# Kernel tuning notes

Measured on AMD Instinct MI355X. Metric: run time of the kernel, lower is better.

The kernel has to match this reference:

```python
import jax, jax.numpy as jnp
import numpy as np

EPS = 1e-6
INV_T = 100.0
STEPS = 7  # eval_steps


def setup_inputs() -> dict:
    key = jax.random.key(0)
    k1, k2 = jax.random.split(key)
    B, C, H, W, R = 8, 512, 128, 128, 64
    x = jax.random.uniform(k1, (B, C, H, W), dtype=jnp.float32)
    bases = jax.random.uniform(k2, (B, C, R), dtype=jnp.float32)
    # _build_bases: F.normalize(bases, dim=1) -> L2 normalize over D
    bases = bases / jnp.maximum(jnp.linalg.norm(bases, axis=1, keepdims=True), 1e-12)
    return {"x": x, "bases": bases}


def _nmf(xf, bases):
    # xf: [B, D, N], bases: [B, D, R]
    # coef init: softmax(inv_t * x^T @ bases) over R
    coef = jax.nn.softmax(INV_T * jnp.einsum('bdn,bdr->bnr', xf, bases), axis=-1)

    def step(carry, _):
        bases, coef = carry
        # multiplicative update for coef: coef * (x^T B) / (coef (B^T B))
        num = jnp.einsum('bdn,bdr->bnr', xf, bases)          # [B,N,R]
        den = coef @ (jnp.swapaxes(bases, 1, 2) @ bases)      # [B,N,R]
        coef = coef * num / (den + EPS)
        # multiplicative update for bases: B * (x coef) / (B (coef^T coef))
        num = jnp.einsum('bdn,bnr->bdr', xf, coef)            # [B,D,R]
        den = bases @ (jnp.swapaxes(coef, 1, 2) @ coef)       # [B,D,R]
        bases = bases * num / (den + EPS)
        return (bases, coef), None

    (bases, coef), _ = jax.lax.scan(step, (bases, coef), None, length=STEPS)
    # compute_coef: one final coef update
    num = jnp.einsum('bdn,bdr->bnr', xf, bases)
    den = coef @ (jnp.swapaxes(bases, 1, 2) @ bases)
    coef = coef * num / (den + EPS)
    return bases, coef


def reference(x, bases):
    B, C, H, W = x.shape
    N = H * W
    xf = x.reshape(B, C, N)  # S=1, D=C
    bases, coef = _nmf(xf, bases)
    out = jnp.einsum('bdr,bnr->bdn', bases, coef)  # bases @ coef^T
    return out.reshape(B, C, H, W)
```

## Files before the change

kernel.cpp:

```cpp
#include <hip/hip_runtime.h>
#include <cstdint>
#include <cstddef>

namespace {

constexpr int B_ = 8;
constexpr int D_ = 512;
constexpr int N_ = 16384;
constexpr int R_ = 64;
constexpr float EPS_ = 1e-6f;
constexpr float INVT_ = 100.0f;

typedef __attribute__((ext_vector_type(4))) float f32x4;
typedef __attribute__((ext_vector_type(8))) short s16x8;
typedef __attribute__((ext_vector_type(4))) short s16x4;

#define MFMA16(A, Bv, C) __builtin_amdgcn_mfma_f32_16x16x32_bf16(A, Bv, C, 0, 0, 0)

#define VMW(n) asm volatile("s_waitcnt vmcnt(" #n ")" ::: "memory")
#define LGKM0 asm volatile("s_waitcnt lgkmcnt(0)" ::: "memory")
#define SCHEDB __builtin_amdgcn_sched_barrier(0)
#define BARRIER do { SCHEDB; __builtin_amdgcn_s_barrier(); SCHEDB; } while (0)

typedef __attribute__((address_space(3))) unsigned int lds_u32_t;
typedef const __attribute__((address_space(1))) unsigned int glb_u32_t;

__device__ __forceinline__ void gl2lds16(const void* g, void* l) {
    __builtin_amdgcn_global_load_lds((glb_u32_t*)g, (lds_u32_t*)l, 16, 0, 0);
}

__device__ __forceinline__ unsigned short f2bf(float x) {
    unsigned int u = __float_as_uint(x);
    return (unsigned short)((u + 0x7fffu + ((u >> 16) & 1u)) >> 16);
}
__device__ __forceinline__ float bf2f(unsigned short u) {
    return __uint_as_float(((unsigned int)u) << 16);
}
__device__ __forceinline__ s16x8 ld8(const unsigned short* p) {
    return *reinterpret_cast<const s16x8*>(p);
}

__device__ __forceinline__ void stage16(const unsigned short* __restrict__ rowbase,
        size_t rstride_elems, unsigned short* __restrict__ buf, int w, int lane) {
#pragma unroll
    for (int i = 0; i < 4; ++i) {
        int r = w * 4 + i;
        const char* src = reinterpret_cast<const char*>(rowbase + (size_t)r * rstride_elems)
                        + ((lane << 4) ^ ((r & 7) << 4));
        gl2lds16(src, reinterpret_cast<char*>(buf) + r * 1024);
    }
}
__device__ __forceinline__ s16x8 read_t16(const unsigned short* buf, int row, int ks, int h4) {
    return *reinterpret_cast<const s16x8*>(reinterpret_cast<const char*>(buf)
        + row * 1024 + ((ks * 64 + h4 * 16) ^ ((row & 7) << 4)));
}
__device__ __forceinline__ void stage_c16(const unsigned short* __restrict__ cnr_n0,
        unsigned short* __restrict__ buf, int w, int lane) {
    int h = w & 1;
    int row = h * 8 + (lane >> 3);
    const char* src = reinterpret_cast<const char*>(cnr_n0 + (size_t)row * R_)
                    + ((((lane & 7) ^ (row & 7))) << 4);
    gl2lds16(src, reinterpret_cast<char*>(buf) + h * 1024);
}
__device__ __forceinline__ s16x8 read_c16(const unsigned short* buf, int row, int ks, int h4) {
    return *reinterpret_cast<const s16x8*>(reinterpret_cast<const char*>(buf)
        + row * 128 + ((ks * 64 + h4 * 16) ^ ((row & 7) << 4)));
}
__device__ __forceinline__ float read_c_scalar(const unsigned short* buf, int row, int r) {
    return bf2f(*reinterpret_cast<const unsigned short*>(
        reinterpret_cast<const char*>(buf) + row * 128 + ((r * 2) ^ ((row & 7) << 4))));
}

__global__ __launch_bounds__(256) void k_convert(const float* __restrict__ X,
        unsigned short* __restrict__ Xhi, unsigned short* __restrict__ XThi,
        unsigned short* __restrict__ XTlo, int have_lo) {
    __shared__ f32x4 lds4[64 * 16];
    int id = blockIdx.x;
    int nblk = id & 255, dblk = (id >> 8) & 7, b = id >> 11;
    int t = threadIdx.x;
    int d = t >> 2, c0 = (t & 3) * 16;
    const float* Xb = X + ((size_t)b * D_ + dblk * 64) * N_ + (size_t)nblk * 64;
    f32x4 v[4];
#pragma unroll
    for (int i = 0; i < 4; ++i)
        v[i] = *reinterpret_cast<const f32x4*>(Xb + (size_t)d * N_ + c0 + 4 * i);
    {
        int swz = (d ^ (d >> 3)) & 7;
#pragma unroll
        for (int i = 0; i < 4; ++i)
            lds4[d * 16 + ((((t & 3) << 2) + i) ^ swz)] = v[i];
    }
    {
        int dfull = dblk * 64 + d;
        int n0 = nblk * 64 + c0;
        unsigned short* dst = Xhi + (size_t)b * D_ * N_
                            + ((size_t)((dfull >> 4) * 32 + (n0 >> 9))) * 8192
                            + (dfull & 15) * 512 + (n0 & 511);
        s16x8 h0, h1;
#pragma unroll
        for (int k = 0; k < 8; ++k) {
            h0[k] = (short)f2bf(v[k >> 2][k & 3]);
            h1[k] = (short)f2bf(v[2 + (k >> 2)][k & 3]);
        }
        *reinterpret_cast<s16x8*>(dst) = h0;
        *reinterpret_cast<s16x8*>(dst + 8) = h1;
    }
    __syncthreads();
    {
        int n = t >> 2;
        const float* L = reinterpret_cast<const float*>(lds4);
        s16x8 h0, h1, l0, l1;
#pragma unroll
        for (int k = 0; k < 16; ++k) {
            int r = c0 + k;
            int sz = (r ^ (r >> 3)) & 7;
            float a = L[r * 64 + ((((n >> 2) ^ sz) << 2) | (n & 3))];
            unsigned short ha = f2bf(a);
            unsigned short la = f2bf(a - bf2f(ha));
            if (k < 8) { h0[k] = (short)ha; l0[k] = (short)la; }
            else       { h1[k - 8] = (short)ha; l1[k - 8] = (short)la; }
        }
        size_t off = ((size_t)b * N_ + nblk * 64 + n) * D_ + dblk * 64 + c0;
        *reinterpret_cast<s16x8*>(XThi + off) = h0;
        *reinterpret_cast<s16x8*>(XThi + off + 8) = h1;
        if (have_lo) {
            *reinterpret_cast<s16x8*>(XTlo + off) = l0;
            *reinterpret_cast<s16x8*>(XTlo + off + 8) = l1;
        }
    }
}

__global__ __launch_bounds__(256) void k_ginit(const float* __restrict__ Bin,
        float* __restrict__ bases, unsigned short* __restrict__ BThi,
        unsigned short* __restrict__ BTlo) {
    __shared__ float lds[64][65];
    int id = blockIdx.x, dblk = id & 7, b = id >> 3;
    int t = threadIdx.x, tn = t & 63, tq = t >> 6;
    const float* Bb = Bin + ((size_t)b * D_ + dblk * 64) * R_;
    float* bb = bases + ((size_t)b * D_ + dblk * 64) * R_;
#pragma unroll
    for (int i = 0; i < 16; ++i) {
        int d = i * 4 + tq;
        float v = Bb[d * R_ + tn];
        lds[d][tn] = v;
        bb[d * R_ + tn] = v;
    }
    __syncthreads();
#pragma unroll
    for (int i = 0; i < 16; ++i) {
        int r = i * 4 + tq;
        float v = lds[tn][r];
        unsigned short hi = f2bf(v);
        size_t off = ((size_t)b * R_ + r) * D_ + dblk * 64 + tn;
        BThi[off] = hi;
        BTlo[off] = f2bf(v - bf2f(hi));
    }
}

__global__ __launch_bounds__(256) void k_gram(const unsigned short* __restrict__ BT,
        unsigned short* __restrict__ G, float* __restrict__ Hf, int zf) {
    int b = blockIdx.x;
    int t = threadIdx.x, lane = t & 63, w = t >> 6;
    int m16 = lane & 15, h4 = lane >> 4;
    if (zf) {
        float* Hz = Hf + (size_t)b * 4096;
#pragma unroll
        for (int i = 0; i < 4; ++i)
            *reinterpret_cast<f32x4*>(Hz + i * 1024 + t * 4) = (f32x4){0.f, 0.f, 0.f, 0.f};
    }
    const unsigned short* BTb = BT + (size_t)b * R_ * D_;
    f32x4 acc[4];
#pragma unroll
    for (int j = 0; j < 4; ++j) acc[j] = (f32x4){0.f, 0.f, 0.f, 0.f};
#pragma unroll
    for (int k0 = 0; k0 < D_; k0 += 32) {
        int kg = k0 + (h4 << 3);
        s16x8 frag[4];
#pragma unroll
        for (int j = 0; j < 4; ++j)
            frag[j] = ld8(BTb + (size_t)(j * 16 + m16) * D_ + kg);
        s16x8 fw = ld8(BTb + (size_t)(w * 16 + m16) * D_ + kg);
#pragma unroll
        for (int j = 0; j < 4; ++j) acc[j] = MFMA16(fw, frag[j], acc[j]);
    }
    unsigned short* Gb = G + (size_t)b * R_ * R_;
#pragma unroll
    for (int j = 0; j < 4; ++j)
#pragma unroll
        for (int q = 0; q < 4; ++q) {
            int r1 = 16 * w + (h4 << 2) + q;
            Gb[r1 * R_ + 16 * j + m16] = f2bf(acc[j][q]);
        }
}

template <int LO>
__global__ __launch_bounds__(256, 2) void k_init(const unsigned short* __restrict__ XThi,
        const unsigned short* __restrict__ XTlo, const unsigned short* __restrict__ BThi,
        const unsigned short* __restrict__ BTlo, const unsigned short* __restrict__ G,
        unsigned short* __restrict__ CTb, unsigned short* __restrict__ Cnr) {
    __shared__ __align__(16) unsigned short xhbuf[2][16 * 512];
    __shared__ __align__(16) unsigned short xlbuf[LO ? 2 : 1][16 * 512];
    __shared__ __align__(16) unsigned short ldsc[16 * 64];
    __shared__ float red[2][4][16];
    int id = blockIdx.x, blk = id & 63, b = id >> 6;
    int t = threadIdx.x, lane = t & 63, w = t >> 6;
    int m16 = lane & 15, h4 = lane >> 4;
    const unsigned short* XTb = XThi + (size_t)b * N_ * D_;
    const unsigned short* XLb = XTlo + (size_t)b * N_ * D_;
    const unsigned short* BThb = BThi + (size_t)b * R_ * D_;
    const unsigned short* BTlb = BTlo + (size_t)b * R_ * D_;
    const unsigned short* Gb = G + (size_t)b * R_ * R_;
    unsigned short* CTbb = CTb + (size_t)b * R_ * N_;
    unsigned short* Cnrb = Cnr + (size_t)b * N_ * R_;
    s16x8 abh[16], abl[16], g[2];
#pragma unroll
    for (int ks = 0; ks < 16; ++ks) {
        size_t off = (size_t)(w * 16 + m16) * D_ + ks * 32 + h4 * 8;
        abh[ks] = ld8(BThb + off);
        abl[ks] = ld8(BTlb + off);
    }
#pragma unroll
    for (int ks = 0; ks < 2; ++ks)
        g[ks] = ld8(Gb + (size_t)(w * 16 + m16) * R_ + ks * 32 + h4 * 8);
    SCHEDB;
    stage16(XTb + (size_t)(blk * 16 + 0) * 16 * D_, D_, xhbuf[0], w, lane);
    if (LO) stage16(XLb + (size_t)(blk * 16 + 0) * 16 * D_, D_, xlbuf[0], w, lane);
    stage16(XTb + (size_t)(blk * 16 + 1) * 16 * D_, D_, xhbuf[1], w, lane);
    if (LO) stage16(XLb + (size_t)(blk * 16 + 1) * 16 * D_, D_, xlbuf[1], w, lane);
    SCHEDB;

    int swz = (m16 & 7) << 4;
    char* crow = reinterpret_cast<char*>(ldsc) + m16 * 128;

    for (int tt = 0; tt < 16; ++tt) {
        int cur = tt & 1;
        int n0 = (blk * 16 + tt) * 16;
        if (LO) {
            if (tt == 0) VMW(8);
            else if (tt == 15) VMW(5);
            else VMW(13);
        } else {
            if (tt == 0) VMW(4);
            else if (tt == 15) VMW(5);
            else VMW(9);
        }
        BARRIER;
        const unsigned short* xh = xhbuf[cur];
        const unsigned short* xl = xlbuf[LO ? cur : 0];
        f32x4 acc = (f32x4){0.f, 0.f, 0.f, 0.f};
#pragma unroll
        for (int ks = 0; ks < 16; ++ks) {
            s16x8 bh = read_t16(xh, m16, ks, h4);
            acc = MFMA16(abh[ks], bh, acc);
            acc = MFMA16(abl[ks], bh, acc);
            if (LO) {
                s16x8 bl = read_t16(xl, m16, ks, h4);
                acc = MFMA16(abh[ks], bl, acc);
            }
        }
        float mx = fmaxf(fmaxf(acc[0], acc[1]), fmaxf(acc[2], acc[3]));
        mx = fmaxf(mx, __shfl_xor(mx, 16));
        mx = fmaxf(mx, __shfl_xor(mx, 32));
        if (lane < 16) red[0][w][m16] = mx;
        LGKM0; BARRIER;
        mx = fmaxf(fmaxf(red[0][0][m16], red[0][1][m16]),
                   fmaxf(red[0][2][m16], red[0][3][m16]));
        float p[4], ss = 0.f;
#pragma unroll
        for (int q = 0; q < 4; ++q) {
            p[q] = __expf(INVT_ * (acc[q] - mx));
            ss += p[q];
        }
        ss += __shfl_xor(ss, 16);
        ss += __shfl_xor(ss, 32);
        if (lane < 16) red[1][w][m16] = ss;
        LGKM0; BARRIER;
        ss = red[1][0][m16] + red[1][1][m16] + red[1][2][m16] + red[1][3][m16];
        float inv = 1.f / ss;
#pragma unroll
        for (int q = 0; q < 4; ++q) {
            int r = w * 16 + h4 * 4 + q;
            *reinterpret_cast<unsigned short*>(crow + ((r * 2) ^ swz)) = f2bf(p[q] * inv);
        }
        LGKM0; BARRIER;
        f32x4 dacc = (f32x4){0.f, 0.f, 0.f, 0.f};
#pragma unroll
        for (int ks = 0; ks < 2; ++ks) {
            s16x8 bf = *reinterpret_cast<const s16x8*>(crow + ((ks * 64 + h4 * 16) ^ swz));
            dacc = MFMA16(g[ks], bf, dacc);
        }
        s16x4 cn;
        float c1v[4];
#pragma unroll
        for (int q = 0; q < 4; ++q) {
            c1v[q] = p[q] * inv * acc[q] / (dacc[q] + EPS_);
            cn[q] = (short)f2bf(c1v[q]);
        }
        LGKM0; BARRIER;
        SCHEDB;
#pragma unroll
        for (int q = 0; q < 4; ++q)
            CTbb[(size_t)(w * 16 + h4 * 4 + q) * N_ + n0 + m16] = f2bf(c1v[q]);
        *reinterpret_cast<s16x4*>(Cnrb + (size_t)(n0 + m16) * R_ + w * 16 + h4 * 4) = cn;
        SCHEDB;
        if (tt + 2 < 16) {
            stage16(XTb + (size_t)(blk * 16 + tt + 2) * 16 * D_, D_, xhbuf[cur], w, lane);
            if (LO) stage16(XLb + (size_t)(blk * 16 + tt + 2) * 16 * D_, D_, xlbuf[cur], w, lane);
        }
        SCHEDB;
    }
}

__global__ __launch_bounds__(256, 4) void k_cu(const unsigned short* __restrict__ XThi,
        const unsigned short* __restrict__ BThi, const unsigned short* __restrict__ G,
        unsigned short* __restrict__ CTb, unsigned short* __restrict__ Cnr) {
    __shared__ __align__(16) unsigned short xbuf[2][16 * 512];
    __shared__ __align__(16) unsigned short cbuf[2][16 * 64];
    int id = blockIdx.x, blk = id & 127, b = id >> 7;
    int t = threadIdx.x, lane = t & 63, w = t >> 6;
    int m16 = lane & 15, h4 = lane >> 4;
    const unsigned short* XTb = XThi + (size_t)b * N_ * D_;
    const unsigned short* BTb = BThi + (size_t)b * R_ * D_;
    const unsigned short* Gb = G + (size_t)b * R_ * R_;
    unsigned short* CTbb = CTb + (size_t)b * R_ * N_;
    unsigned short* Cnrb = Cnr + (size_t)b * N_ * R_;
    s16x8 abt[16], g[2];
#pragma unroll
    for (int ks = 0; ks < 16; ++ks)
        abt[ks] = ld8(BTb + (size_t)(w * 16 + m16) * D_ + ks * 32 + h4 * 8);
#pragma unroll
    for (int ks = 0; ks < 2; ++ks)
        g[ks] = ld8(Gb + (size_t)(w * 16 + m16) * R_ + ks * 32 + h4 * 8);
    SCHEDB;
    stage16(XTb + (size_t)(blk * 8 + 0) * 16 * D_, D_, xbuf[0], w, lane);
    stage_c16(Cnrb + (size_t)(blk * 8 + 0) * 16 * R_, cbuf[0], w, lane);
    stage16(XTb + (size_t)(blk * 8 + 1) * 16 * D_, D_, xbuf[1], w, lane);
    stage_c16(Cnrb + (size_t)(blk * 8 + 1) * 16 * R_, cbuf[1], w, lane);
    SCHEDB;

    for (int tt = 0; tt < 8; ++tt) {
        int cur = tt & 1;
        int n0 = (blk * 8 + tt) * 16;
        if (tt == 0) VMW(5);
        else if (tt == 7) VMW(5);
        else VMW(10);
        BARRIER;
        const unsigned short* xb = xbuf[cur];
        const unsigned short* cb = cbuf[cur];
        f32x4 acc = (f32x4){0.f, 0.f, 0.f, 0.f};
#pragma unroll
        for (int ks = 0; ks < 16; ++ks)
            acc = MFMA16(abt[ks], read_t16(xb, m16, ks, h4), acc);
        f32x4 dacc = (f32x4){0.f, 0.f, 0.f, 0.f};
#pragma unroll
        for (int ks = 0; ks < 2; ++ks)
            dacc = MFMA16(g[ks], read_c16(cb, m16, ks, h4), dacc);
        s16x4 cn;
        float c1v[4];
#pragma unroll
        for (int q = 0; q < 4; ++q) {
            int r = w * 16 + h4 * 4 + q;
            float cold = read_c_scalar(cb, m16, r);
            c1v[q] = cold * acc[q] / (dacc[q] + EPS_);
            cn[q] = (short)f2bf(c1v[q]);
        }
        LGKM0; BARRIER;
        SCHEDB;
#pragma unroll
        for (int q = 0; q < 4; ++q)
            CTbb[(size_t)(w * 16 + h4 * 4 + q) * N_ + n0 + m16] = f2bf(c1v[q]);
        *reinterpret_cast<s16x4*>(Cnrb + (size_t)(n0 + m16) * R_ + w * 16 + h4 * 4) = cn;
        SCHEDB;
        if (tt + 2 < 8) {
            stage16(XTb + (size_t)(blk * 8 + tt + 2) * 16 * D_, D_, xbuf[cur], w, lane);
            stage_c16(Cnrb + (size_t)(blk * 8 + tt + 2) * 16 * R_, cbuf[cur], w, lane);
        }
        SCHEDB;
    }
}

__global__ __launch_bounds__(256, 4) void k_bu1t(const unsigned short* __restrict__ Xhi,
        const unsigned short* __restrict__ CTb, unsigned short* __restrict__ wsN2,
        float* __restrict__ Hf, int sp) {
    __shared__ __align__(16) unsigned short xbuf[2][16 * 512];
    int id = blockIdx.x;
    int b = id >> 7, c = (id >> 2) & 31, dg = id & 3;
    int t = threadIdx.x, lane = t & 63, w = t >> 6;
    int m16 = lane & 15, h4 = lane >> 4;
    const unsigned short* Xb = Xhi + (size_t)b * D_ * N_;
    const unsigned short* Cbc = CTb + (size_t)b * R_ * N_ + c * 512;
    s16x8 act[16];
#pragma unroll
    for (int ks = 0; ks < 16; ++ks)
        act[ks] = ld8(Cbc + (size_t)(w * 16 + m16) * N_ + ks * 32 + h4 * 8);
    SCHEDB;
    stage16(Xb + ((size_t)((dg * 8 + 0) * 32 + c)) * 8192, 512, xbuf[0], w, lane);
    stage16(Xb + ((size_t)((dg * 8 + 1) * 32 + c)) * 8192, 512, xbuf[1], w, lane);
    SCHEDB;
    f32x4 hacc = (f32x4){0.f, 0.f, 0.f, 0.f};
    {
        const unsigned short* Hrow = Cbc + (size_t)(dg * 16 + m16) * N_;
#pragma unroll
        for (int gg = 0; gg < 4; ++gg) {
            SCHEDB;
            s16x8 hb[4];
#pragma unroll
            for (int j = 0; j < 4; ++j)
                hb[j] = ld8(Hrow + (gg * 4 + j) * 32 + h4 * 8);
#pragma unroll
            for (int j = 0; j < 4; ++j)
                hacc = MFMA16(act[gg * 4 + j], hb[j], hacc);
        }
    }
    SCHEDB;
    unsigned short* n2 = wsN2 + (size_t)(b * 32 + c) * R_ * D_;
    for (int tt = 0; tt < 8; ++tt) {
        int cur = tt & 1;
        int d0 = dg * 128 + tt * 16;
        if (tt == 0) VMW(4);
        else if (tt == 7) VMW(4);
        else VMW(8);
        BARRIER;
        const unsigned short* xb = xbuf[cur];
        f32x4 acc = (f32x4){0.f, 0.f, 0.f, 0.f};
#pragma unroll
        for (int ks = 0; ks < 16; ++ks)
            acc = MFMA16(act[ks], read_t16(xb, m16, ks, h4), acc);
        LGKM0; BARRIER;
        SCHEDB;
        if (tt + 2 < 8)
            stage16(Xb + ((size_t)((dg * 8 + tt + 2) * 32 + c)) * 8192, 512, xbuf[cur], w, lane);
        SCHEDB;
#pragma unroll
        for (int q = 0; q < 4; ++q)
            n2[(size_t)(w * 16 + h4 * 4 + q) * D_ + d0 + m16] = f2bf(acc[q]);
        SCHEDB;
    }
    float* Hfb = Hf + (size_t)sp * (B_ * 4096) + (size_t)b * 4096;
#pragma unroll
    for (int q = 0; q < 4; ++q)
        atomicAdd(&Hfb[(w * 16 + h4 * 4 + q) * R_ + dg * 16 + m16], hacc[q]);
}

__global__ __launch_bounds__(256) void k_bu2(const unsigned short* __restrict__ wsN2,
        float* __restrict__ Hf, int sp, float* __restrict__ bases,
        unsigned short* __restrict__ BThi, unsigned short* __restrict__ Bdr) {
    __shared__ float ldsH[64][64];
    __shared__ float ldsb[16][65];
    __shared__ float ldsn[16][65];
    int id = blockIdx.x, dblk = id & 31, b = id >> 5;
    int t = threadIdx.x;
    int d0 = dblk * 16;
    {
        float* Hz = Hf + (size_t)(1 - sp) * (B_ * 4096) + (size_t)id * 128;
        if (t < 32) *reinterpret_cast<f32x4*>(Hz + t * 4) = (f32x4){0.f, 0.f, 0.f, 0.f};
    }
    const float* Hb = Hf + (size_t)sp * (B_ * 4096) + (size_t)b * 4096;
#pragma unroll
    for (int i = 0; i < 4; ++i) {
        f32x4 v = *reinterpret_cast<const f32x4*>(Hb + i * 1024 + t * 4);
        *reinterpret_cast<f32x4*>(&ldsH[0][0] + i * 1024 + t * 4) = v;
    }
    {
        int d = t >> 4, p0 = (t & 15) * 4;
        f32x4 v = *reinterpret_cast<const f32x4*>(bases + ((size_t)b * D_ + d0 + d) * R_ + p0);
#pragma unroll
        for (int k = 0; k < 4; ++k) ldsb[d][p0 + k] = v[k];
    }
    __syncthreads();
#pragma unroll
    for (int j = 0; j < 4; ++j) {
        int i = t + 256 * j;
        int r = i >> 4, d = i & 15;
        float n2 = 0.f;
        for (int c = 0; c < 32; ++c)
            n2 += bf2f(wsN2[(((size_t)b * 32 + c) * R_ + r) * D_ + d0 + d]);
        float den = 0.f;
#pragma unroll 8
        for (int p = 0; p < 64; ++p) den += ldsb[d][p] * ldsH[p][r];
        ldsn[d][r] = ldsb[d][r] * n2 / (den + EPS_);
    }
    __syncthreads();
    {
        int d = t >> 4, r0 = (t & 15) * 4;
        f32x4 v;
        s16x4 hv;
#pragma unroll
        for (int k = 0; k < 4; ++k) {
            v[k] = ldsn[d][r0 + k];
            hv[k] = (short)f2bf(v[k]);
        }
        *reinterpret_cast<f32x4*>(bases + ((size_t)b * D_ + d0 + d) * R_ + r0) = v;
        *reinterpret_cast<s16x4*>((unsigned short*)Bdr + ((size_t)b * D_ + d0 + d) * R_ + r0) = hv;
    }
    {
        int r = t >> 2, dd = (t & 3) * 4;
        s16x4 hv;
#pragma unroll
        for (int k = 0; k < 4; ++k) hv[k] = (short)f2bf(ldsn[dd + k][r]);
        *reinterpret_cast<s16x4*>(BThi + ((size_t)b * R_ + r) * D_ + d0 + dd) = hv;
    }
}

__global__ __launch_bounds__(256, 2) void k_out(const unsigned short* __restrict__ Bdr,
        const unsigned short* __restrict__ Cnr, float* __restrict__ Out) {
    __shared__ float ldso[4][64 * 68 + 8];
    int id = blockIdx.x, nblk = id & 63, dblk = (id >> 6) & 7, b = id >> 9;
    int t = threadIdx.x, lane = t & 63, w = t >> 6;
    int m16 = lane & 15, h4 = lane >> 4;
    const unsigned short* Bb = Bdr + (size_t)b * D_ * R_;
    const unsigned short* Cb = Cnr + (size_t)b * N_ * R_;
    int d0 = dblk * 64, n0 = nblk * 256 + w * 64;
    f32x4 acc[4][4];
#pragma unroll
    for (int i = 0; i < 4; ++i)
#pragma unroll
        for (int j = 0; j < 4; ++j) acc[i][j] = (f32x4){0.f, 0.f, 0.f, 0.f};
#pragma unroll
    for (int k0 = 0; k0 < 64; k0 += 32) {
        int kg = k0 + (h4 << 3);
        s16x8 afrag[4], bfrag[4];
#pragma unroll
        for (int i = 0; i < 4; ++i)
            afrag[i] = ld8(Bb + (size_t)(d0 + i * 16 + m16) * R_ + kg);
#pragma unroll
        for (int j = 0; j < 4; ++j)
            bfrag[j] = ld8(Cb + (size_t)(n0 + j * 16 + m16) * R_ + kg);
#pragma unroll
        for (int i = 0; i < 4; ++i)
#pragma unroll
            for (int j = 0; j < 4; ++j)
                acc[i][j] = MFMA16(afrag[i], bfrag[j], acc[i][j]);
    }
#pragma unroll
    for (int i = 0; i < 4; ++i)
#pragma unroll
        for (int j = 0; j < 4; ++j)
#pragma unroll
            for (int q = 0; q < 4; ++q)
                ldso[w][(i * 16 + h4 * 4 + q) * 68 + j * 16 + m16] = acc[i][j][q];
    __syncthreads();
    float* Ob = Out + (size_t)b * D_ * N_ + (size_t)d0 * N_ + nblk * 256;
    int quad = lane >> 4, cc = (lane & 15) * 4;
#pragma unroll
    for (int i = 0; i < 16; ++i) {
        int d = w * 16 + i;
        f32x4 v = *reinterpret_cast<const f32x4*>(&ldso[quad][d * 68 + cc]);
        *reinterpret_cast<f32x4*>(Ob + (size_t)d * N_ + quad * 64 + cc) = v;
    }
}

}

extern "C" void kernel_launch(void* const* d_in, const int* in_sizes, int n_in,
                              void* d_out, int out_size, void* d_ws, size_t ws_size,
                              hipStream_t stream) {
    const float* X = (const float*)d_in[0];
    const float* Bin = (const float*)d_in[1];
    float* Out = (float*)d_out;
    char* ws = (char*)d_ws;

    const size_t o_Xhi  = 0;
    const size_t o_XThi = o_Xhi  + (size_t)B_ * D_ * N_ * 2;
    const size_t o_CTb  = o_XThi + (size_t)B_ * N_ * D_ * 2;
    const size_t o_Cnr  = o_CTb  + (size_t)B_ * R_ * N_ * 2;
    const size_t o_bas  = o_Cnr  + (size_t)B_ * N_ * R_ * 2;
    const size_t o_BThi = o_bas  + (size_t)B_ * D_ * R_ * 4;
    const size_t o_BTlo = o_BThi + (size_t)B_ * R_ * D_ * 2;
    const size_t o_Bdr  = o_BTlo + (size_t)B_ * R_ * D_ * 2;
    const size_t o_G    = o_Bdr  + (size_t)B_ * D_ * R_ * 2;
    const size_t o_Hf   = o_G    + (size_t)B_ * R_ * R_ * 2;
    const size_t o_N2   = o_Hf   + (size_t)2 * B_ * R_ * R_ * 4;
    const size_t BASE   = o_N2   + (size_t)B_ * 32 * R_ * D_ * 2;
    const size_t o_XTlo = BASE;
    const size_t FULL   = o_XTlo + (size_t)B_ * N_ * D_ * 2;

    if (ws_size < BASE) return;
    int have_lo = ws_size >= FULL ? 1 : 0;

    unsigned short* Xhi  = (unsigned short*)(ws + o_Xhi);
    unsigned short* XThi = (unsigned short*)(ws + o_XThi);
    unsigned short* XTlo = (unsigned short*)(ws + (have_lo ? o_XTlo : o_XThi));
    unsigned short* CTb  = (unsigned short*)(ws + o_CTb);
    unsigned short* Cnr  = (unsigned short*)(ws + o_Cnr);
    float*          bas  = (float*)(ws + o_bas);
    unsigned short* BThi = (unsigned short*)(ws + o_BThi);
    unsigned short* BTlo = (unsigned short*)(ws + o_BTlo);
    unsigned short* Bdr  = (unsigned short*)(ws + o_Bdr);
    unsigned short* G    = (unsigned short*)(ws + o_G);
    float*          Hf   = (float*)(ws + o_Hf);
    unsigned short* N2   = (unsigned short*)(ws + o_N2);

    k_convert<<<dim3(16384), dim3(256), 0, stream>>>(X, Xhi, XThi, XTlo, have_lo);
    k_ginit<<<dim3(64), dim3(256), 0, stream>>>(Bin, bas, BThi, BTlo);
    k_gram<<<dim3(8), dim3(256), 0, stream>>>(BThi, G, Hf, 1);
    if (have_lo)
        k_init<1><<<dim3(512), dim3(256), 0, stream>>>(XThi, XTlo, BThi, BTlo, G, CTb, Cnr);
    else
        k_init<0><<<dim3(512), dim3(256), 0, stream>>>(XThi, XTlo, BThi, BTlo, G, CTb, Cnr);
    for (int s = 0; s < 7; ++s) {
        int sp = s & 1;
        k_bu1t<<<dim3(1024), dim3(256), 0, stream>>>(Xhi, CTb, N2, Hf, sp);
        k_bu2<<<dim3(256), dim3(256), 0, stream>>>(N2, Hf, sp, bas, BThi, Bdr);
        k_gram<<<dim3(8), dim3(256), 0, stream>>>(BThi, G, Hf, 0);
        k_cu<<<dim3(1024), dim3(256), 0, stream>>>(XThi, BThi, G, CTb, Cnr);
    }
    k_out<<<dim3(4096), dim3(256), 0, stream>>>(Bdr, Cnr, Out);
}
```

Baseline: 1.172 ms.

## Fuse Gram matrix computation into bases update via fp32 atomic partial sums

Removes the separate 8-block k_gram launch inside the iteration loop. Each k_bu2 block now computes a 16-row partial of B^T B in fp32 from the freshly updated bases held in LDS and atomically adds it into a double-buffered fp32 Gram buffer. k_cu reads that buffer and converts it to bf16 itself. This saves a serial, poorly parallel launch per step, at the cost of many global atomics in k_bu2 and the extra buffer zeroing.

```diff
diff --git a/kernel.cpp b/kernel.cpp
--- a/kernel.cpp
+++ b/kernel.cpp
@@ -158,15 +158,19 @@
 }
 
 __global__ __launch_bounds__(256) void k_gram(const unsigned short* __restrict__ BT,
-        unsigned short* __restrict__ G, float* __restrict__ Hf, int zf) {
+        unsigned short* __restrict__ G, float* __restrict__ Hf, float* __restrict__ Gf,
+        int zf) {
     int b = blockIdx.x;
     int t = threadIdx.x, lane = t & 63, w = t >> 6;
     int m16 = lane & 15, h4 = lane >> 4;
     if (zf) {
         float* Hz = Hf + (size_t)b * 4096;
-#pragma unroll
-        for (int i = 0; i < 4; ++i)
+        float* Gz = Gf + (size_t)b * 4096;
+#pragma unroll
+        for (int i = 0; i < 4; ++i) {
             *reinterpret_cast<f32x4*>(Hz + i * 1024 + t * 4) = (f32x4){0.f, 0.f, 0.f, 0.f};
+            *reinterpret_cast<f32x4*>(Gz + i * 1024 + t * 4) = (f32x4){0.f, 0.f, 0.f, 0.f};
+        }
     }
     const unsigned short* BTb = BT + (size_t)b * R_ * D_;
     f32x4 acc[4];
@@ -312,7 +316,7 @@
 }
 
 __global__ __launch_bounds__(256, 4) void k_cu(const unsigned short* __restrict__ XThi,
-        const unsigned short* __restrict__ BThi, const unsigned short* __restrict__ G,
+        const unsigned short* __restrict__ BThi, const float* __restrict__ Gf, int sp,
         unsigned short* __restrict__ CTb, unsigned short* __restrict__ Cnr) {
     __shared__ __align__(16) unsigned short xbuf[2][16 * 512];
     __shared__ __align__(16) unsigned short cbuf[2][16 * 64];
@@ -321,7 +325,7 @@
     int m16 = lane & 15, h4 = lane >> 4;
     const unsigned short* XTb = XThi + (size_t)b * N_ * D_;
     const unsigned short* BTb = BThi + (size_t)b * R_ * D_;
-    const unsigned short* Gb = G + (size_t)b * R_ * R_;
+    const float* Gfb = Gf + (size_t)sp * (B_ * 4096) + (size_t)b * 4096;
     unsigned short* CTbb = CTb + (size_t)b * R_ * N_;
     unsigned short* Cnrb = Cnr + (size_t)b * N_ * R_;
     s16x8 abt[16], g[2];
@@ -329,8 +333,16 @@
     for (int ks = 0; ks < 16; ++ks)
         abt[ks] = ld8(BTb + (size_t)(w * 16 + m16) * D_ + ks * 32 + h4 * 8);
 #pragma unroll
-    for (int ks = 0; ks < 2; ++ks)
-        g[ks] = ld8(Gb + (size_t)(w * 16 + m16) * R_ + ks * 32 + h4 * 8);
+    for (int ks = 0; ks < 2; ++ks) {
+        const float* gp = Gfb + (w * 16 + m16) * R_ + ks * 32 + h4 * 8;
+        f32x4 g0 = *reinterpret_cast<const f32x4*>(gp);
+        f32x4 g1 = *reinterpret_cast<const f32x4*>(gp + 4);
+#pragma unroll
+        for (int k = 0; k < 4; ++k) {
+            g[ks][k]     = (short)f2bf(g0[k]);
+            g[ks][k + 4] = (short)f2bf(g1[k]);
+        }
+    }
     SCHEDB;
     stage16(XTb + (size_t)(blk * 8 + 0) * 16 * D_, D_, xbuf[0], w, lane);
     stage_c16(Cnrb + (size_t)(blk * 8 + 0) * 16 * R_, cbuf[0], w, lane);
@@ -443,7 +455,7 @@
 }
 
 __global__ __launch_bounds__(256) void k_bu2(const unsigned short* __restrict__ wsN2,
-        float* __restrict__ Hf, int sp, float* __restrict__ bases,
+        float* __restrict__ Hf, float* __restrict__ Gf, int sp, float* __restrict__ bases,
         unsigned short* __restrict__ BThi, unsigned short* __restrict__ Bdr) {
     __shared__ float ldsH[64][64];
     __shared__ float ldsb[16][65];
@@ -453,7 +465,11 @@
     int d0 = dblk * 16;
     {
         float* Hz = Hf + (size_t)(1 - sp) * (B_ * 4096) + (size_t)id * 128;
-        if (t < 32) *reinterpret_cast<f32x4*>(Hz + t * 4) = (f32x4){0.f, 0.f, 0.f, 0.f};
+        float* Gz = Gf + (size_t)(1 - sp) * (B_ * 4096) + (size_t)id * 128;
+        if (t < 32) {
+            *reinterpret_cast<f32x4*>(Hz + t * 4) = (f32x4){0.f, 0.f, 0.f, 0.f};
+            *reinterpret_cast<f32x4*>(Gz + t * 4) = (f32x4){0.f, 0.f, 0.f, 0.f};
+        }
     }
     const float* Hb = Hf + (size_t)sp * (B_ * 4096) + (size_t)b * 4096;
 #pragma unroll
@@ -500,6 +516,20 @@
         for (int k = 0; k < 4; ++k) hv[k] = (short)f2bf(ldsn[dd + k][r]);
         *reinterpret_cast<s16x4*>(BThi + ((size_t)b * R_ + r) * D_ + d0 + dd) = hv;
     }
+    {
+        int r1 = t >> 2, r2b = (t & 3) * 16;
+        float a[16];
+#pragma unroll
+        for (int d = 0; d < 16; ++d) a[d] = ldsn[d][r1];
+        float* Gfb = Gf + (size_t)sp * (B_ * 4096) + (size_t)b * 4096;
+#pragma unroll
+        for (int j = 0; j < 16; ++j) {
+            float s = 0.f;
+#pragma unroll
+            for (int d = 0; d < 16; ++d) s += a[d] * ldsn[d][r2b + j];
+            atomicAdd(&Gfb[r1 * R_ + r2b + j], s);
+        }
+    }
 }
 
 __global__ __launch_bounds__(256, 2) void k_out(const unsigned short* __restrict__ Bdr,
@@ -570,7 +600,8 @@
     const size_t o_Bdr  = o_BTlo + (size_t)B_ * R_ * D_ * 2;
     const size_t o_G    = o_Bdr  + (size_t)B_ * D_ * R_ * 2;
     const size_t o_Hf   = o_G    + (size_t)B_ * R_ * R_ * 2;
-    const size_t o_N2   = o_Hf   + (size_t)2 * B_ * R_ * R_ * 4;
+    const size_t o_Gf   = o_Hf   + (size_t)2 * B_ * R_ * R_ * 4;
+    const size_t o_N2   = o_Gf   + (size_t)2 * B_ * R_ * R_ * 4;
     const size_t BASE   = o_N2   + (size_t)B_ * 32 * R_ * D_ * 2;
     const size_t o_XTlo = BASE;
     const size_t FULL   = o_XTlo + (size_t)B_ * N_ * D_ * 2;
@@ -589,11 +620,12 @@
     unsigned short* Bdr  = (unsigned short*)(ws + o_Bdr);
     unsigned short* G    = (unsigned short*)(ws + o_G);
     float*          Hf   = (float*)(ws + o_Hf);
+    float*          Gf   = (float*)(ws + o_Gf);
     unsigned short* N2   = (unsigned short*)(ws + o_N2);
 
     k_convert<<<dim3(16384), dim3(256), 0, stream>>>(X, Xhi, XThi, XTlo, have_lo);
     k_ginit<<<dim3(64), dim3(256), 0, stream>>>(Bin, bas, BThi, BTlo);
-    k_gram<<<dim3(8), dim3(256), 0, stream>>>(BThi, G, Hf, 1);
+    k_gram<<<dim3(8), dim3(256), 0, stream>>>(BThi, G, Hf, Gf, 1);
     if (have_lo)
         k_init<1><<<dim3(512), dim3(256), 0, stream>>>(XThi, XTlo, BThi, BTlo, G, CTb, Cnr);
     else
@@ -601,9 +633,8 @@
     for (int s = 0; s < 7; ++s) {
         int sp = s & 1;
         k_bu1t<<<dim3(1024), dim3(256), 0, stream>>>(Xhi, CTb, N2, Hf, sp);
-        k_bu2<<<dim3(256), dim3(256), 0, stream>>>(N2, Hf, sp, bas, BThi, Bdr);
-        k_gram<<<dim3(8), dim3(256), 0, stream>>>(BThi, G, Hf, 0);
-        k_cu<<<dim3(1024), dim3(256), 0, stream>>>(XThi, BThi, G, CTb, Cnr);
+        k_bu2<<<dim3(256), dim3(256), 0, stream>>>(N2, Hf, Gf, sp, bas, BThi, Bdr);
+        k_cu<<<dim3(1024), dim3(256), 0, stream>>>(XThi, BThi, Gf, sp, CTb, Cnr);
     }
     k_out<<<dim3(4096), dim3(256), 0, stream>>>(Bdr, Cnr, Out);
 }
```

Measured after the change: 1.432 ms. +22.1%, slower.
